# Performance work log

Hardware: AMD Instinct MI355X
Metric: run time of the kernel (lower is better)

Reference implementation:

```python
import jax, jax.numpy as jnp
import numpy as np

TEMPERATURE = 1.0
TOP_K = 50
TOP_P = 0.95
NEG_INF = float('-inf')


def setup_inputs() -> dict:
    key = jax.random.key(0)
    k1, k2, k3, k4 = jax.random.split(key, 4)
    B, S, D, V = 32, 8, 1024, 50257
    psi_real = jax.random.normal(k1, (B, S, D), dtype=jnp.float32)
    psi_imag = jax.random.normal(k2, (B, S, D), dtype=jnp.float32)
    W_real = jax.random.normal(k3, (V, D), dtype=jnp.float32) * 0.02
    W_imag = jax.random.normal(k4, (V, D), dtype=jnp.float32) * 0.02
    bias = jnp.zeros((V,), dtype=jnp.float32)
    return {"psi_real": psi_real, "psi_imag": psi_imag, "W_real": W_real,
            "W_imag": W_imag, "bias": bias}


def _legacy_filter(logits, temperature, top_k, top_p):
    # temperature
    l = logits / max(temperature, 1e-8)
    # top-k: keep values >= k-th largest
    if 0 < top_k < l.shape[-1]:
        topk_vals = jax.lax.top_k(l, top_k)[0]          # [B,S,k]
        threshold = topk_vals[..., -1:]
        l = jnp.where(l < threshold, NEG_INF, l)
    # top-p (nucleus): mask tokens where exclusive cumulative prob >= p
    if top_p < 1.0:
        p = max(top_p, 1e-6)
        order = jnp.argsort(-l, axis=-1)                # descending
        sl = jnp.take_along_axis(l, order, axis=-1)
        sp = jax.nn.softmax(sl, axis=-1)
        cum = jnp.cumsum(sp, axis=-1)
        mask = (cum - sp) >= p                          # exclusive cumsum >= p
        mask = mask.at[..., 0].set(False)               # always keep top token
        sl = jnp.where(mask, NEG_INF, sl)
        inv = jnp.argsort(order, axis=-1)               # scatter back to original order
        l = jnp.take_along_axis(sl, inv, axis=-1)
    return l


def reference(psi_real, psi_imag, W_real, W_imag, bias):
    # logits = proj_real(psi.real) + proj_imag(psi.imag) + bias  -> [B,S,V]
    logits = (jnp.einsum('bsd,vd->bsv', psi_real, W_real)
              + jnp.einsum('bsd,vd->bsv', psi_imag, W_imag) + bias)
    sampling_logits = _legacy_filter(logits, TEMPERATURE, TOP_K, TOP_P)
    probs = jax.nn.softmax(sampling_logits, axis=-1)
    # multinomial(probs, 1) == categorical over filtered logits
    tokens = jax.random.categorical(jax.random.key(42), sampling_logits, axis=-1)
    log_probs = jax.nn.log_softmax(logits, axis=-1)
    return logits, tokens, probs, log_probs
```

## Files before the change

kernel.cpp:

```cpp
#include <hip/hip_runtime.h>
#include <stdint.h>
#include <math.h>

#define MM 256
#define KD 1024
#define K2 2048
#define VV 50257
#define NF4 (VV / 4)
#define ROWQ (NF4 + 1)

static constexpr size_t OUT_TOKENS = (size_t)MM * VV;
static constexpr size_t OUT_PROBS  = OUT_TOKENS + MM;
static constexpr size_t OUT_LOGPR  = OUT_PROBS + (size_t)MM * VV;

#define WS_ABUF_BYTES (2u * 1024u * 1024u)

typedef __attribute__((ext_vector_type(8))) short bf16x8;
typedef __attribute__((ext_vector_type(4))) float f32x4;

__device__ __forceinline__ ushort f2bf(float x) {
  unsigned u = __float_as_uint(x);
  unsigned r = u + 0x7FFFu + ((u >> 16) & 1u);
  return (ushort)(r >> 16);
}
__device__ __forceinline__ float bf2f(ushort h) {
  return __uint_as_float(((unsigned)h) << 16);
}

__device__ __forceinline__ unsigned rotl32(unsigned x, int r) {
  return (x << r) | (x >> (32 - r));
}

__device__ __forceinline__ uint2 threefry2x32(unsigned k0, unsigned k1,
                                              unsigned x0, unsigned x1) {
  unsigned ks[3] = {k0, k1, k0 ^ k1 ^ 0x1BD11BDAu};
  const int rot[8] = {13, 15, 26, 6, 17, 29, 16, 24};
  x0 += ks[0]; x1 += ks[1];
  #pragma unroll
  for (int g = 0; g < 5; ++g) {
    const int base = (g & 1) ? 4 : 0;
    #pragma unroll
    for (int i = 0; i < 4; ++i) {
      x0 += x1;
      x1 = rotl32(x1, rot[base + i]);
      x1 ^= x0;
    }
    x0 += ks[(g + 1) % 3];
    x1 += ks[(g + 2) % 3] + (unsigned)(g + 1);
  }
  return make_uint2(x0, x1);
}

__device__ __forceinline__ float gumbel_at(unsigned flat) {
  uint2 r = threefry2x32(0u, 42u, 0u, flat);
  unsigned w = r.x ^ r.y;
  unsigned fb = (w >> 9) | 0x3F800000u;
  float f = __uint_as_float(fb) - 1.0f;
  const float tiny = 1.1754943508222875e-38f;
  float u = fmaxf(tiny, f + tiny);
  float t1 = (float)log((double)u);
  float t3 = (float)log((double)(-t1));
  return -t3;
}

__global__ __launch_bounds__(256)
void k_prep(const float* __restrict__ psi_r, const float* __restrict__ psi_i,
            ushort* __restrict__ a_buf) {
  int t = blockIdx.x * 256 + threadIdx.x;
  int lane = t & 63;
  int mb = (t >> 6) & 15;
  int s = t >> 10;
  int lr = lane & 15, lg = lane >> 4;
  int m = mb * 16 + lr;
  int kloc = (s & 31) * 32 + lg * 8;
  const float* __restrict__ src = (s < 32) ? psi_r : psi_i;
  float4 v0 = *reinterpret_cast<const float4*>(&src[m * KD + kloc]);
  float4 v1 = *reinterpret_cast<const float4*>(&src[m * KD + kloc + 4]);
  float in[8] = {v0.x, v0.y, v0.z, v0.w, v1.x, v1.y, v1.z, v1.w};
  ushort h[8], l[8];
  #pragma unroll
  for (int j = 0; j < 8; ++j) {
    h[j] = f2bf(in[j]);
    l[j] = f2bf(in[j] - bf2f(h[j]));
  }
  size_t base = ((size_t)(s * 16 + mb) * 2) * 512 + (size_t)lane * 8;
  #pragma unroll
  for (int j = 0; j < 8; ++j) {
    a_buf[base + j] = h[j];
    a_buf[base + 512 + j] = l[j];
  }
}

#define BN 64
#define BK 64
#define GT 512

__global__ __launch_bounds__(GT, 4)
void k_gemm(const uint4* __restrict__ a_buf,
            const float* __restrict__ Wr, const float* __restrict__ Wi,
            const float* __restrict__ bias, float* __restrict__ logits) {
  __shared__ ushort sBh[2][BN * BK];
  __shared__ ushort sBl[2][BN * BK];

  const int tid  = threadIdx.x;
  const int lane = tid & 63;
  const int wid  = tid >> 6;
  const int vb   = blockIdx.x * BN;
  const int lr = lane & 15;
  const int lg = lane >> 4;

  const int brow = tid >> 3;
  const int bc8  = (tid & 7) << 3;
  const int gn   = vb + brow;
  const int eoW  = brow * BK + (bc8 ^ ((brow & 7) << 3));

  f32x4 acc[2][4];
  #pragma unroll
  for (int i = 0; i < 2; ++i)
    #pragma unroll
    for (int j = 0; j < 4; ++j)
      #pragma unroll
      for (int q = 0; q < 4; ++q) acc[i][j][q] = 0.f;

  float4 wa = make_float4(0.f, 0.f, 0.f, 0.f), wb = wa;
  if (gn < VV) {
    wa = *reinterpret_cast<const float4*>(&Wr[(size_t)gn * KD + bc8]);
    wb = *reinterpret_cast<const float4*>(&Wr[(size_t)gn * KD + bc8 + 4]);
  }

  int cur = 0;
  for (int s2 = 0; s2 < K2 / BK; ++s2) {
    uint4 vah[2][2], val[2][2];
    #pragma unroll
    for (int kq = 0; kq < 2; ++kq) {
      #pragma unroll
      for (int mi = 0; mi < 2; ++mi) {
        int chunk2 = (((s2 * 2 + kq) * 16) + wid * 2 + mi) * 2;
        vah[kq][mi] = a_buf[(size_t)chunk2 * 64 + lane];
        val[kq][mi] = a_buf[(size_t)(chunk2 + 1) * 64 + lane];
      }
    }
    {
      float in[8] = {wa.x, wa.y, wa.z, wa.w, wb.x, wb.y, wb.z, wb.w};
      ushort h[8], l[8];
      #pragma unroll
      for (int j = 0; j < 8; ++j) {
        h[j] = f2bf(in[j]);
        l[j] = f2bf(in[j] - bf2f(h[j]));
      }
      *reinterpret_cast<uint4*>(&sBh[cur][eoW]) =
          make_uint4((unsigned)h[0] | ((unsigned)h[1] << 16),
                     (unsigned)h[2] | ((unsigned)h[3] << 16),
                     (unsigned)h[4] | ((unsigned)h[5] << 16),
                     (unsigned)h[6] | ((unsigned)h[7] << 16));
      *reinterpret_cast<uint4*>(&sBl[cur][eoW]) =
          make_uint4((unsigned)l[0] | ((unsigned)l[1] << 16),
                     (unsigned)l[2] | ((unsigned)l[3] << 16),
                     (unsigned)l[4] | ((unsigned)l[5] << 16),
                     (unsigned)l[6] | ((unsigned)l[7] << 16));
    }
    if (s2 < K2 / BK - 1) {
      int kk = (s2 + 1) * BK;
      const float* __restrict__ Bs = (kk < KD) ? Wr : Wi;
      int ko = kk & (KD - 1);
      if (gn < VV) {
        wa = *reinterpret_cast<const float4*>(&Bs[(size_t)gn * KD + ko + bc8]);
        wb = *reinterpret_cast<const float4*>(&Bs[(size_t)gn * KD + ko + bc8 + 4]);
      }
    }
    asm volatile("s_waitcnt lgkmcnt(0)" ::: "memory");
    asm volatile("s_barrier" ::: "memory");

    #pragma unroll
    for (int kq = 0; kq < 2; ++kq) {
      bf16x8 bh[4], bl[4];
      #pragma unroll
      for (int ni = 0; ni < 4; ++ni) {
        int r = ni * 16 + lr;
        int eoff = r * BK + ((kq * 32 + lg * 8) ^ ((r & 7) << 3));
        bh[ni] = *reinterpret_cast<const bf16x8*>(&sBh[cur][eoff]);
        bl[ni] = *reinterpret_cast<const bf16x8*>(&sBl[cur][eoff]);
      }
      #pragma unroll
      for (int mi = 0; mi < 2; ++mi) {
        bf16x8 ah = *reinterpret_cast<bf16x8*>(&vah[kq][mi]);
        bf16x8 al = *reinterpret_cast<bf16x8*>(&val[kq][mi]);
        #pragma unroll
        for (int ni = 0; ni < 4; ++ni) {
          acc[mi][ni] = __builtin_amdgcn_mfma_f32_16x16x32_bf16(ah, bh[ni], acc[mi][ni], 0, 0, 0);
          acc[mi][ni] = __builtin_amdgcn_mfma_f32_16x16x32_bf16(al, bh[ni], acc[mi][ni], 0, 0, 0);
          acc[mi][ni] = __builtin_amdgcn_mfma_f32_16x16x32_bf16(ah, bl[ni], acc[mi][ni], 0, 0, 0);
        }
      }
    }
    cur ^= 1;
  }

  #pragma unroll
  for (int ni = 0; ni < 4; ++ni) {
    int n = vb + ni * 16 + lr;
    if (n < VV) {
      float b = bias[n];
      #pragma unroll
      for (int mi = 0; mi < 2; ++mi) {
        #pragma unroll
        for (int j = 0; j < 4; ++j) {
          int m = wid * 32 + mi * 16 + lg * 4 + j;
          logits[(size_t)m * VV + n] = acc[mi][ni][j] + b;
        }
      }
    }
  }
}

__device__ __forceinline__ unsigned ordf(float f) {
  unsigned u = __float_as_uint(f);
  return u ^ ((u >> 31) ? 0xFFFFFFFFu : 0x80000000u);
}

#define HREP 4
#define HSTRIDE 4097

__global__ __launch_bounds__(1024)
void k_stats(const float* __restrict__ logits, float* __restrict__ ws4) {
  const int row = blockIdx.x;
  const int tid = threadIdx.x;
  const float* __restrict__ x = logits + (size_t)row * VV;

  __shared__ unsigned hist[HREP * HSTRIDE];
  __shared__ float pm[16], ps[16];

  for (int i = tid; i < HREP * HSTRIDE; i += 1024) hist[i] = 0u;
  __syncthreads();

  const int rep = (tid & 3) * HSTRIDE;
  float lm = -INFINITY, ls = 0.f;
  for (int i4 = tid; i4 < NF4; i4 += 1024) {
    float4 v4 = *reinterpret_cast<const float4*>(&x[i4 * 4]);
    float vs[4] = {v4.x, v4.y, v4.z, v4.w};
    #pragma unroll
    for (int j = 0; j < 4; ++j) {
      float v = vs[j];
      atomicAdd(&hist[rep + (ordf(v) >> 20)], 1u);
      if (v <= lm) {
        ls += expf(v - lm);
      } else {
        ls = ls * expf(lm - v) + 1.f;
        lm = v;
      }
    }
  }
  if (tid == 0) {
    float v = x[VV - 1];
    atomicAdd(&hist[ordf(v) >> 20], 1u);
    if (v <= lm) ls += expf(v - lm);
    else { ls = ls * expf(lm - v) + 1.f; lm = v; }
  }
  #pragma unroll
  for (int off = 32; off; off >>= 1) {
    float om = __shfl_xor(lm, off);
    float os = __shfl_xor(ls, off);
    float M = fmaxf(lm, om);
    ls = ls * expf(lm - M) + os * expf(om - M);
    lm = M;
  }
  if ((tid & 63) == 0) { pm[tid >> 6] = lm; ps[tid >> 6] = ls; }
  __syncthreads();

  for (int b = tid; b < 4096; b += 1024)
    hist[b] = hist[b] + hist[HSTRIDE + b] + hist[2 * HSTRIDE + b] + hist[3 * HSTRIDE + b];
  __syncthreads();

  if (tid < 64) {
    float m2 = (tid < 16) ? pm[tid] : -3e38f;
    float s2 = (tid < 16) ? ps[tid] : 0.f;
    #pragma unroll
    for (int off = 8; off; off >>= 1) {
      float om = __shfl_xor(m2, off);
      float os = __shfl_xor(s2, off);
      float M = fmaxf(m2, om);
      s2 = s2 * expf(m2 - M) + os * expf(om - M);
      m2 = M;
    }
    unsigned seg = 0;
    #pragma unroll 8
    for (int b = 0; b < 64; ++b) seg += hist[tid * 64 + ((b + tid) & 63)];
    unsigned suf = seg;
    #pragma unroll
    for (int off = 1; off < 64; off <<= 1) {
      unsigned o = __shfl_down(suf, off);
      if (tid + off < 64) suf += o;
    }
    unsigned long long mk = __ballot(suf >= 50u);
    int lstar = 63 - __builtin_clzll(mk);
    unsigned above = (lstar < 63) ? (unsigned)__shfl((int)suf, lstar + 1) : 0u;
    if (tid == 0) {
      unsigned cum = above;
      int bin = lstar * 64;
      for (int b = 63; b >= 0; --b) {
        cum += hist[lstar * 64 + b];
        if (cum >= 50u) { bin = lstar * 64 + b; break; }
      }
      ws4[row * 4 + 0] = m2;
      ws4[row * 4 + 1] = logf(s2);
      ws4[row * 4 + 2] = __uint_as_float((unsigned)bin << 20);
    }
  }
}

__global__ __launch_bounds__(1024)
void k_logprobs(const float* __restrict__ logits, const float* __restrict__ ws4,
                float* __restrict__ logpr, float* __restrict__ probs) {
  const int totq = MM * ROWQ;
  for (int q = blockIdx.x * blockDim.x + threadIdx.x; q < totq;
       q += gridDim.x * blockDim.x) {
    unsigned row = (unsigned)q / (unsigned)ROWQ;
    unsigned c = (unsigned)q - row * ROWQ;
    float mx = ws4[row * 4 + 0], lz = ws4[row * 4 + 1];
    size_t base = (size_t)row * VV;
    if (c < NF4) {
      size_t idx = base + c * 4;
      float4 v = *reinterpret_cast<const float4*>(&logits[idx]);
      *reinterpret_cast<float4*>(&logpr[idx]) =
          make_float4((v.x - mx) - lz, (v.y - mx) - lz,
                      (v.z - mx) - lz, (v.w - mx) - lz);
      *reinterpret_cast<float4*>(&probs[idx]) = make_float4(0.f, 0.f, 0.f, 0.f);
    } else {
      size_t idx = base + VV - 1;
      logpr[idx] = (logits[idx] - mx) - lz;
      probs[idx] = 0.f;
    }
  }
}

#define CAP 1024

__global__ __launch_bounds__(1024)
void k_collect(const float* __restrict__ logits, const float* __restrict__ ws4,
               float* __restrict__ probs, float* __restrict__ tokens) {
  const int row = blockIdx.x;
  const int tid = threadIdx.x;
  const float* __restrict__ x = logits + (size_t)row * VV;

  __shared__ float cv[CAP];
  __shared__ int   ci[CAP];
  __shared__ unsigned s_cnt;
  __shared__ float top_v[50];
  __shared__ int   top_i[50];

  if (tid == 0) s_cnt = 0u;
  __syncthreads();

  const unsigned lo = __float_as_uint(ws4[row * 4 + 2]);
  for (int i4 = tid; i4 < NF4; i4 += 1024) {
    float4 v = *reinterpret_cast<const float4*>(&x[i4 * 4]);
    float vs[4] = {v.x, v.y, v.z, v.w};
    #pragma unroll
    for (int j = 0; j < 4; ++j) {
      if (ordf(vs[j]) >= lo) {
        unsigned pos = atomicAdd(&s_cnt, 1u);
        if (pos < CAP) { cv[pos] = vs[j]; ci[pos] = i4 * 4 + j; }
      }
    }
  }
  if (tid == 0) {
    float v = x[VV - 1];
    if (ordf(v) >= lo) {
      unsigned pos = atomicAdd(&s_cnt, 1u);
      if (pos < CAP) { cv[pos] = v; ci[pos] = VV - 1; }
    }
  }
  __syncthreads();
  const int ncand = (int)min(s_cnt, (unsigned)CAP);

  if (tid < 64) {
    for (int it = 0; it < 50; ++it) {
      float bv = -INFINITY;
      int bi = 0x7FFFFFFF, bs = 0;
      for (int c = tid; c < ncand; c += 64) {
        float v = cv[c];
        int id = ci[c];
        if (v > bv || (v == bv && id < bi)) { bv = v; bi = id; bs = c; }
      }
      #pragma unroll
      for (int off = 32; off; off >>= 1) {
        float ov = __shfl_xor(bv, off);
        int oi = __shfl_xor(bi, off);
        int os = __shfl_xor(bs, off);
        if (ov > bv || (ov == bv && oi < bi)) { bv = ov; bi = oi; bs = os; }
      }
      if (tid == 0) {
        top_v[it] = bv;
        top_i[it] = bi;
        cv[bs] = -INFINITY;
      }
    }

    float tv = (tid < 50) ? top_v[tid] : -3e38f;
    float mx = top_v[0];
    float sp = (tid < 50) ? expf(tv - mx) : 0.f;
    float Z = sp;
    #pragma unroll
    for (int off = 32; off; off >>= 1) Z += __shfl_xor(Z, off);
    float pref = sp;
    #pragma unroll
    for (int off = 1; off < 64; off <<= 1) {
      float o = __shfl_up(pref, off);
      if (tid >= off) pref += o;
    }
    float excl = (pref - sp) / Z;
    bool keep = (tid < 50) && ((tid == 0) || (excl < 0.95f));
    float spk = keep ? sp : 0.f;
    float Z2 = spk;
    #pragma unroll
    for (int off = 32; off; off >>= 1) Z2 += __shfl_xor(Z2, off);

    float bt = -3e38f;
    int bidx = 0x7FFFFFFF;
    if (keep) {
      int idx = top_i[tid];
      probs[(size_t)row * VV + idx] = sp / Z2;
      bt = tv + gumbel_at((unsigned)((size_t)row * VV + idx));
      bidx = idx;
    }
    #pragma unroll
    for (int off = 32; off; off >>= 1) {
      float ot = __shfl_xor(bt, off);
      int oi = __shfl_xor(bidx, off);
      if (ot > bt || (ot == bt && oi < bidx)) { bt = ot; bidx = oi; }
    }
    if (tid == 0) tokens[row] = (float)bidx;
  }
}

extern "C" void kernel_launch(void* const* d_in, const int* in_sizes, int n_in,
                              void* d_out, int out_size, void* d_ws, size_t ws_size,
                              hipStream_t stream) {
  const float* psi_r = (const float*)d_in[0];
  const float* psi_i = (const float*)d_in[1];
  const float* Wr    = (const float*)d_in[2];
  const float* Wi    = (const float*)d_in[3];
  const float* bias  = (const float*)d_in[4];
  float* out = (float*)d_out;

  ushort* a_buf = (ushort*)d_ws;
  float* ws4    = (float*)((char*)d_ws + WS_ABUF_BYTES);

  float* logits = out;
  float* tokens = out + OUT_TOKENS;
  float* probs  = out + OUT_PROBS;
  float* logpr  = out + OUT_LOGPR;

  k_prep<<<256, 256, 0, stream>>>(psi_r, psi_i, a_buf);
  const int nblk = (VV + BN - 1) / BN;
  k_gemm<<<nblk, GT, 0, stream>>>((const uint4*)a_buf, Wr, Wi, bias, logits);
  k_stats<<<MM, 1024, 0, stream>>>(logits, ws4);
  k_logprobs<<<2048, 1024, 0, stream>>>(logits, ws4, logpr, probs);
  k_collect<<<MM, 1024, 0, stream>>>(logits, ws4, probs, tokens);
}
```

Baseline: 287.9 us.

## Widen GEMM per-wave M tile, add MFMA priority, fuse logprob into collect

The GEMM block drops from 512 to 256 threads. Each wave now covers 64 rows of M instead of 32, so every B fragment read from LDS feeds twice as many MFMAs. Each thread also converts 16 W elements per stage instead of 8. s_setprio is raised around the MFMA loop. The separate log-softmax/zero-probs kernel is merged into the per-row collect kernel, which saves one launch and one extra read of the logits. The costs are higher register pressure, fewer waves per block, and lower occupancy for the post-processing pass, which now runs only one block per row.

```diff
diff --git a/kernel.cpp b/kernel.cpp
--- a/kernel.cpp
+++ b/kernel.cpp
@@ -7,7 +7,6 @@
 #define K2 2048
 #define VV 50257
 #define NF4 (VV / 4)
-#define ROWQ (NF4 + 1)
 
 static constexpr size_t OUT_TOKENS = (size_t)MM * VV;
 static constexpr size_t OUT_PROBS  = OUT_TOKENS + MM;
@@ -93,9 +92,9 @@
 
 #define BN 64
 #define BK 64
-#define GT 512
-
-__global__ __launch_bounds__(GT, 4)
+#define GT 256
+
+__global__ __launch_bounds__(GT, 2)
 void k_gemm(const uint4* __restrict__ a_buf,
             const float* __restrict__ Wr, const float* __restrict__ Wi,
             const float* __restrict__ bias, float* __restrict__ logits) {
@@ -109,63 +108,81 @@
   const int lr = lane & 15;
   const int lg = lane >> 4;
 
-  const int brow = tid >> 3;
-  const int bc8  = (tid & 7) << 3;
+  const int brow = tid >> 2;
+  const int bcol = (tid & 3) << 4;
   const int gn   = vb + brow;
-  const int eoW  = brow * BK + (bc8 ^ ((brow & 7) << 3));
-
-  f32x4 acc[2][4];
-  #pragma unroll
-  for (int i = 0; i < 2; ++i)
+  const int eo0  = brow * BK + (bcol ^ ((brow & 7) << 3));
+  const int eo1  = brow * BK + ((bcol + 8) ^ ((brow & 7) << 3));
+
+  f32x4 acc[4][4];
+  #pragma unroll
+  for (int i = 0; i < 4; ++i)
     #pragma unroll
     for (int j = 0; j < 4; ++j)
       #pragma unroll
       for (int q = 0; q < 4; ++q) acc[i][j][q] = 0.f;
 
-  float4 wa = make_float4(0.f, 0.f, 0.f, 0.f), wb = wa;
+  float4 w0 = make_float4(0.f, 0.f, 0.f, 0.f), w1 = w0, w2 = w0, w3 = w0;
   if (gn < VV) {
-    wa = *reinterpret_cast<const float4*>(&Wr[(size_t)gn * KD + bc8]);
-    wb = *reinterpret_cast<const float4*>(&Wr[(size_t)gn * KD + bc8 + 4]);
+    const float* p = &Wr[(size_t)gn * KD + bcol];
+    w0 = *reinterpret_cast<const float4*>(p);
+    w1 = *reinterpret_cast<const float4*>(p + 4);
+    w2 = *reinterpret_cast<const float4*>(p + 8);
+    w3 = *reinterpret_cast<const float4*>(p + 12);
   }
 
   int cur = 0;
   for (int s2 = 0; s2 < K2 / BK; ++s2) {
-    uint4 vah[2][2], val[2][2];
+    uint4 vah[2][4], val[2][4];
     #pragma unroll
     for (int kq = 0; kq < 2; ++kq) {
       #pragma unroll
-      for (int mi = 0; mi < 2; ++mi) {
-        int chunk2 = (((s2 * 2 + kq) * 16) + wid * 2 + mi) * 2;
+      for (int mi = 0; mi < 4; ++mi) {
+        int chunk2 = (((s2 * 2 + kq) * 16) + wid * 4 + mi) * 2;
         vah[kq][mi] = a_buf[(size_t)chunk2 * 64 + lane];
         val[kq][mi] = a_buf[(size_t)(chunk2 + 1) * 64 + lane];
       }
     }
     {
-      float in[8] = {wa.x, wa.y, wa.z, wa.w, wb.x, wb.y, wb.z, wb.w};
-      ushort h[8], l[8];
-      #pragma unroll
-      for (int j = 0; j < 8; ++j) {
+      float in[16] = {w0.x, w0.y, w0.z, w0.w, w1.x, w1.y, w1.z, w1.w,
+                      w2.x, w2.y, w2.z, w2.w, w3.x, w3.y, w3.z, w3.w};
+      ushort h[16], l[16];
+      #pragma unroll
+      for (int j = 0; j < 16; ++j) {
         h[j] = f2bf(in[j]);
         l[j] = f2bf(in[j] - bf2f(h[j]));
       }
-      *reinterpret_cast<uint4*>(&sBh[cur][eoW]) =
+      *reinterpret_cast<uint4*>(&sBh[cur][eo0]) =
           make_uint4((unsigned)h[0] | ((unsigned)h[1] << 16),
                      (unsigned)h[2] | ((unsigned)h[3] << 16),
                      (unsigned)h[4] | ((unsigned)h[5] << 16),
                      (unsigned)h[6] | ((unsigned)h[7] << 16));
-      *reinterpret_cast<uint4*>(&sBl[cur][eoW]) =
+      *reinterpret_cast<uint4*>(&sBh[cur][eo1]) =
+          make_uint4((unsigned)h[8] | ((unsigned)h[9] << 16),
+                     (unsigned)h[10] | ((unsigned)h[11] << 16),
+                     (unsigned)h[12] | ((unsigned)h[13] << 16),
+                     (unsigned)h[14] | ((unsigned)h[15] << 16));
+      *reinterpret_cast<uint4*>(&sBl[cur][eo0]) =
           make_uint4((unsigned)l[0] | ((unsigned)l[1] << 16),
                      (unsigned)l[2] | ((unsigned)l[3] << 16),
                      (unsigned)l[4] | ((unsigned)l[5] << 16),
                      (unsigned)l[6] | ((unsigned)l[7] << 16));
+      *reinterpret_cast<uint4*>(&sBl[cur][eo1]) =
+          make_uint4((unsigned)l[8] | ((unsigned)l[9] << 16),
+                     (unsigned)l[10] | ((unsigned)l[11] << 16),
+                     (unsigned)l[12] | ((unsigned)l[13] << 16),
+                     (unsigned)l[14] | ((unsigned)l[15] << 16));
     }
     if (s2 < K2 / BK - 1) {
       int kk = (s2 + 1) * BK;
       const float* __restrict__ Bs = (kk < KD) ? Wr : Wi;
       int ko = kk & (KD - 1);
       if (gn < VV) {
-        wa = *reinterpret_cast<const float4*>(&Bs[(size_t)gn * KD + ko + bc8]);
-        wb = *reinterpret_cast<const float4*>(&Bs[(size_t)gn * KD + ko + bc8 + 4]);
+        const float* p = &Bs[(size_t)gn * KD + ko + bcol];
+        w0 = *reinterpret_cast<const float4*>(p);
+        w1 = *reinterpret_cast<const float4*>(p + 4);
+        w2 = *reinterpret_cast<const float4*>(p + 8);
+        w3 = *reinterpret_cast<const float4*>(p + 12);
       }
     }
     asm volatile("s_waitcnt lgkmcnt(0)" ::: "memory");
@@ -181,8 +198,9 @@
         bh[ni] = *reinterpret_cast<const bf16x8*>(&sBh[cur][eoff]);
         bl[ni] = *reinterpret_cast<const bf16x8*>(&sBl[cur][eoff]);
       }
-      #pragma unroll
-      for (int mi = 0; mi < 2; ++mi) {
+      __builtin_amdgcn_s_setprio(1);
+      #pragma unroll
+      for (int mi = 0; mi < 4; ++mi) {
         bf16x8 ah = *reinterpret_cast<bf16x8*>(&vah[kq][mi]);
         bf16x8 al = *reinterpret_cast<bf16x8*>(&val[kq][mi]);
         #pragma unroll
@@ -192,6 +210,7 @@
           acc[mi][ni] = __builtin_amdgcn_mfma_f32_16x16x32_bf16(ah, bl[ni], acc[mi][ni], 0, 0, 0);
         }
       }
+      __builtin_amdgcn_s_setprio(0);
     }
     cur ^= 1;
   }
@@ -202,10 +221,10 @@
     if (n < VV) {
       float b = bias[n];
       #pragma unroll
-      for (int mi = 0; mi < 2; ++mi) {
+      for (int mi = 0; mi < 4; ++mi) {
         #pragma unroll
         for (int j = 0; j < 4; ++j) {
-          int m = wid * 32 + mi * 16 + lg * 4 + j;
+          int m = wid * 64 + mi * 16 + lg * 4 + j;
           logits[(size_t)m * VV + n] = acc[mi][ni][j] + b;
         }
       }
@@ -308,39 +327,17 @@
   }
 }
 
+#define CAP 1024
+
 __global__ __launch_bounds__(1024)
-void k_logprobs(const float* __restrict__ logits, const float* __restrict__ ws4,
-                float* __restrict__ logpr, float* __restrict__ probs) {
-  const int totq = MM * ROWQ;
-  for (int q = blockIdx.x * blockDim.x + threadIdx.x; q < totq;
-       q += gridDim.x * blockDim.x) {
-    unsigned row = (unsigned)q / (unsigned)ROWQ;
-    unsigned c = (unsigned)q - row * ROWQ;
-    float mx = ws4[row * 4 + 0], lz = ws4[row * 4 + 1];
-    size_t base = (size_t)row * VV;
-    if (c < NF4) {
-      size_t idx = base + c * 4;
-      float4 v = *reinterpret_cast<const float4*>(&logits[idx]);
-      *reinterpret_cast<float4*>(&logpr[idx]) =
-          make_float4((v.x - mx) - lz, (v.y - mx) - lz,
-                      (v.z - mx) - lz, (v.w - mx) - lz);
-      *reinterpret_cast<float4*>(&probs[idx]) = make_float4(0.f, 0.f, 0.f, 0.f);
-    } else {
-      size_t idx = base + VV - 1;
-      logpr[idx] = (logits[idx] - mx) - lz;
-      probs[idx] = 0.f;
-    }
-  }
-}
-
-#define CAP 1024
-
-__global__ __launch_bounds__(1024)
-void k_collect(const float* __restrict__ logits, const float* __restrict__ ws4,
-               float* __restrict__ probs, float* __restrict__ tokens) {
+void k_post(const float* __restrict__ logits, const float* __restrict__ ws4,
+            float* __restrict__ logpr, float* __restrict__ probs,
+            float* __restrict__ tokens) {
   const int row = blockIdx.x;
   const int tid = threadIdx.x;
   const float* __restrict__ x = logits + (size_t)row * VV;
+  float* __restrict__ lp = logpr + (size_t)row * VV;
+  float* __restrict__ pr = probs + (size_t)row * VV;
 
   __shared__ float cv[CAP];
   __shared__ int   ci[CAP];
@@ -351,9 +348,17 @@
   if (tid == 0) s_cnt = 0u;
   __syncthreads();
 
+  const float mx = ws4[row * 4 + 0];
+  const float lz = ws4[row * 4 + 1];
   const unsigned lo = __float_as_uint(ws4[row * 4 + 2]);
+  const float4 z4 = make_float4(0.f, 0.f, 0.f, 0.f);
+
   for (int i4 = tid; i4 < NF4; i4 += 1024) {
     float4 v = *reinterpret_cast<const float4*>(&x[i4 * 4]);
+    *reinterpret_cast<float4*>(&lp[i4 * 4]) =
+        make_float4((v.x - mx) - lz, (v.y - mx) - lz,
+                    (v.z - mx) - lz, (v.w - mx) - lz);
+    *reinterpret_cast<float4*>(&pr[i4 * 4]) = z4;
     float vs[4] = {v.x, v.y, v.z, v.w};
     #pragma unroll
     for (int j = 0; j < 4; ++j) {
@@ -365,6 +370,8 @@
   }
   if (tid == 0) {
     float v = x[VV - 1];
+    lp[VV - 1] = (v - mx) - lz;
+    pr[VV - 1] = 0.f;
     if (ordf(v) >= lo) {
       unsigned pos = atomicAdd(&s_cnt, 1u);
       if (pos < CAP) { cv[pos] = v; ci[pos] = VV - 1; }
@@ -397,8 +404,8 @@
     }
 
     float tv = (tid < 50) ? top_v[tid] : -3e38f;
-    float mx = top_v[0];
-    float sp = (tid < 50) ? expf(tv - mx) : 0.f;
+    float m0 = top_v[0];
+    float sp = (tid < 50) ? expf(tv - m0) : 0.f;
     float Z = sp;
     #pragma unroll
     for (int off = 32; off; off >>= 1) Z += __shfl_xor(Z, off);
@@ -419,7 +426,7 @@
     int bidx = 0x7FFFFFFF;
     if (keep) {
       int idx = top_i[tid];
-      probs[(size_t)row * VV + idx] = sp / Z2;
+      pr[idx] = sp / Z2;
       bt = tv + gumbel_at((unsigned)((size_t)row * VV + idx));
       bidx = idx;
     }
@@ -455,6 +462,5 @@
   const int nblk = (VV + BN - 1) / BN;
   k_gemm<<<nblk, GT, 0, stream>>>((const uint4*)a_buf, Wr, Wi, bias, logits);
   k_stats<<<MM, 1024, 0, stream>>>(logits, ws4);
-  k_logprobs<<<2048, 1024, 0, stream>>>(logits, ws4, logpr, probs);
-  k_collect<<<MM, 1024, 0, stream>>>(logits, ws4, probs, tokens);
-}
+  k_post<<<MM, 1024, 0, stream>>>(logits, ws4, logpr, probs, tokens);
+}
```

New measurement: 285.6 us. No clear change (-0.8%).
